# Kernel tuning notes

Hardware: AMD Instinct MI355X
Metric: run time of the kernel (lower is better)

The kernel has to match this reference:

```python
import jax, jax.numpy as jnp
import numpy as np

DIM = 1024
HEADS = 16
DIM_HEAD = 64
INNER = HEADS * DIM_HEAD  # 1024


def setup_inputs() -> dict:
    key = jax.random.key(0)
    k1, k2, k3, k4 = jax.random.split(key, 4)
    x = jax.random.normal(k1, (4, 2048, DIM), dtype=jnp.float32)
    # nn.Linear(dim, 3*inner, bias=False): weight (3*inner, dim); store transposed (dim, 3*inner)
    w_qkv = jax.random.normal(k2, (DIM, 3 * INNER), dtype=jnp.float32) * (DIM ** -0.5)
    # nn.Linear(inner, dim) with bias
    w_out = jax.random.normal(k3, (INNER, DIM), dtype=jnp.float32) * (INNER ** -0.5)
    b_out = jax.random.normal(k4, (DIM,), dtype=jnp.float32) * 0.01
    return {"x": x, "w_qkv": w_qkv, "w_out": w_out, "b_out": b_out}


def reference(x, w_qkv, w_out, b_out):
    b, n, _ = x.shape
    scale = DIM_HEAD ** -0.5
    qkv = x @ w_qkv  # [b, n, 3*inner]
    q, k, v = jnp.split(qkv, 3, axis=-1)
    # 'b n (h d) -> b h n d'
    def split_heads(t):
        return t.reshape(b, n, HEADS, DIM_HEAD).transpose(0, 2, 1, 3)
    q, k, v = split_heads(q), split_heads(k), split_heads(v)
    sim = jnp.einsum('bhid,bhjd->bhij', q, k) * scale  # [b, h, n, n]
    attn = jax.nn.softmax(sim, axis=-1)
    out = jnp.einsum('bhij,bhjd->bhid', attn, v)  # [b, h, n, d]
    out = out.transpose(0, 2, 1, 3).reshape(b, n, INNER)  # 'b h n d -> b n (h d)'
    return out @ w_out + b_out
```

## Files before the change

### kernel.cpp

```cpp
#include <hip/hip_runtime.h>
#include <hip/hip_bf16.h>

#define BATCH 4
#define SEQ   2048
#define DIM   1024
#define HEADS 16
#define DHEAD 64
#define INNER 1024
#define QKV_N 3072
#define MTOT  8192

typedef short bf16x8 __attribute__((ext_vector_type(8)));
typedef float f32x4  __attribute__((ext_vector_type(4)));
#define MFMA16(a,b,c) __builtin_amdgcn_mfma_f32_16x16x32_bf16((a),(b),(c),0,0,0)

#define QSCALE 0.1803368801111204f

static __device__ __forceinline__ unsigned fau(float f) { return __float_as_uint(f); }
static __device__ __forceinline__ float max3f(float a, float b, float c) {
    return fmaxf(fmaxf(a, b), c);
}

static __device__ __forceinline__ uint2 pack_hi4(float4 v) {
    return make_uint2((fau(v.x) >> 16) | (fau(v.y) & 0xffff0000u),
                      (fau(v.z) >> 16) | (fau(v.w) & 0xffff0000u));
}
static __device__ __forceinline__ float4 resid4(float4 v) {
    float4 r;
    r.x = v.x - __uint_as_float(fau(v.x) & 0xffff0000u);
    r.y = v.y - __uint_as_float(fau(v.y) & 0xffff0000u);
    r.z = v.z - __uint_as_float(fau(v.z) & 0xffff0000u);
    r.w = v.w - __uint_as_float(fau(v.w) & 0xffff0000u);
    return r;
}
static __device__ __forceinline__ uint2 pack_lo4(float4 v) { return pack_hi4(resid4(v)); }

static __device__ __forceinline__ unsigned cvt_pk_bf16(float a, float b) {
    unsigned r;
    asm("v_cvt_pk_bf16_f32 %0, %1, %2" : "=v"(r) : "v"(a), "v"(b));
    return r;
}

static __device__ __forceinline__ void barrier_lgkm() {
    asm volatile("s_waitcnt lgkmcnt(0)" ::: "memory");
    __builtin_amdgcn_s_barrier();
}

static __device__ __forceinline__ void stagger_block() {
    const unsigned flat = blockIdx.x + gridDim.x * (blockIdx.y + gridDim.y * blockIdx.z);
    const int slot = (int)(flat % 5u);
    #pragma unroll
    for (int i = 0; i < 4; ++i)
        if (i < slot) __builtin_amdgcn_s_sleep(6);
}

__global__ __launch_bounds__(256) void pack_rows_hl(const float* __restrict__ src,
                                                    unsigned short* __restrict__ dst,
                                                    int Mtot, int K)
{
    const int m = blockIdx.x * 256 + threadIdx.x;
    const int t = blockIdx.y;
    const float* sp = src + (size_t)m * K + t * 32;
    unsigned short buf[64];
    #pragma unroll
    for (int i = 0; i < 32; i += 4) {
        const float4 v = *(const float4*)&sp[i];
        *(uint2*)&buf[i]      = pack_hi4(v);
        *(uint2*)&buf[32 + i] = pack_lo4(v);
    }
    unsigned short* dp = dst + ((size_t)t * Mtot + m) * 64;
    const int s7 = m & 7;
    #pragma unroll
    for (int G = 0; G < 8; ++G)
        *(bf16x8*)&dp[(G ^ s7) * 8] = *(bf16x8*)&buf[G * 8];
}

__global__ __launch_bounds__(256) void pack_cols_hl(const float* __restrict__ src,
                                                    unsigned short* __restrict__ dst,
                                                    int Ntot)
{
    const int n = blockIdx.x * 256 + threadIdx.x;
    const int t = blockIdx.y;
    float vals[32];
    #pragma unroll
    for (int i = 0; i < 32; ++i) vals[i] = src[(size_t)(t * 32 + i) * Ntot + n];
    unsigned short buf[64];
    #pragma unroll
    for (int i = 0; i < 32; i += 4) {
        const float4 v = make_float4(vals[i], vals[i + 1], vals[i + 2], vals[i + 3]);
        *(uint2*)&buf[i]      = pack_hi4(v);
        *(uint2*)&buf[32 + i] = pack_lo4(v);
    }
    unsigned short* dp = dst + ((size_t)t * Ntot + n) * 64;
    const int s7 = n & 7;
    #pragma unroll
    for (int G = 0; G < 8; ++G)
        *(bf16x8*)&dp[(G ^ s7) * 8] = *(bf16x8*)&buf[G * 8];
}

static __device__ __forceinline__ void gemm_core_pk(const unsigned short* __restrict__ Ap,
                                                    const unsigned short* __restrict__ Bp,
                                                    unsigned short* As,
                                                    unsigned short* Bs,
                                                    f32x4 (&acc)[4][4],
                                                    int Mtot, int Ntot, int NT,
                                                    int row0, int col0)
{
    const int tid  = threadIdx.x;
    const int lane = tid & 63;
    const int w    = tid >> 6;
    const int l15  = lane & 15;
    const int g    = lane >> 4;
    const int wr   = w >> 1, wc = w & 1;

    const unsigned short* aSrc = Ap + (size_t)row0 * 64 + tid * 8;
    const unsigned short* bSrc = Bp + (size_t)col0 * 64 + tid * 8;
    const size_t aStep = (size_t)Mtot * 64;
    const size_t bStep = (size_t)Ntot * 64;

    int aoff[4][2], boff[4][2];
    #pragma unroll
    for (int mt = 0; mt < 4; ++mt) {
        const int m = wr * 64 + mt * 16 + l15;
        const int sw = (m & 7) << 3;
        aoff[mt][0] = m * 64 + ((g * 8) ^ sw);
        aoff[mt][1] = m * 64 + ((32 + g * 8) ^ sw);
    }
    #pragma unroll
    for (int nt = 0; nt < 4; ++nt) {
        const int n = wc * 64 + nt * 16 + l15;
        const int sw = (n & 7) << 3;
        boff[nt][0] = n * 64 + ((g * 8) ^ sw);
        boff[nt][1] = n * 64 + ((32 + g * 8) ^ sw);
    }

    bf16x8 ar[4], br[4];
    #pragma unroll
    for (int p = 0; p < 4; ++p) {
        ar[p] = *(const bf16x8*)(aSrc + p * 2048);
        br[p] = *(const bf16x8*)(bSrc + p * 2048);
    }
    #pragma unroll
    for (int p = 0; p < 4; ++p) {
        *(bf16x8*)&As[tid * 8 + p * 2048] = ar[p];
        *(bf16x8*)&Bs[tid * 8 + p * 2048] = br[p];
    }
    if (1 < NT) {
        #pragma unroll
        for (int p = 0; p < 4; ++p) {
            ar[p] = *(const bf16x8*)(aSrc + aStep + p * 2048);
            br[p] = *(const bf16x8*)(bSrc + bStep + p * 2048);
        }
    }
    __syncthreads();

    int cur = 0;
    for (int t = 0; t < NT; ++t) {
        const int cb = cur * 8192;
        bf16x8 ah[4], al[4], bh[4], bl[4];
        #pragma unroll
        for (int mt = 0; mt < 4; ++mt) {
            ah[mt] = *(const bf16x8*)&As[cb + aoff[mt][0]];
            al[mt] = *(const bf16x8*)&As[cb + aoff[mt][1]];
        }
        #pragma unroll
        for (int nt = 0; nt < 4; ++nt) {
            bh[nt] = *(const bf16x8*)&Bs[cb + boff[nt][0]];
            bl[nt] = *(const bf16x8*)&Bs[cb + boff[nt][1]];
        }
        if (t + 1 < NT) {
            const int nb = (cur ^ 1) * 8192;
            #pragma unroll
            for (int p = 0; p < 4; ++p) {
                *(bf16x8*)&As[nb + tid * 8 + p * 2048] = ar[p];
                *(bf16x8*)&Bs[nb + tid * 8 + p * 2048] = br[p];
            }
        }
        if (t + 2 < NT) {
            const unsigned short* a2 = aSrc + (size_t)(t + 2) * aStep;
            const unsigned short* b2 = bSrc + (size_t)(t + 2) * bStep;
            #pragma unroll
            for (int p = 0; p < 4; ++p) {
                ar[p] = *(const bf16x8*)(a2 + p * 2048);
                br[p] = *(const bf16x8*)(b2 + p * 2048);
            }
        }
        #pragma unroll
        for (int mt = 0; mt < 4; ++mt)
            #pragma unroll
            for (int nt = 0; nt < 4; ++nt) {
                acc[mt][nt] = MFMA16(ah[mt], bh[nt], acc[mt][nt]);
                acc[mt][nt] = MFMA16(ah[mt], bl[nt], acc[mt][nt]);
                acc[mt][nt] = MFMA16(al[mt], bh[nt], acc[mt][nt]);
            }
        barrier_lgkm();
        cur ^= 1;
    }
}

__global__ __launch_bounds__(256, 2) void gemm_out_pk(const unsigned short* __restrict__ Ap,
                                                      const unsigned short* __restrict__ Bp,
                                                      const float* __restrict__ bias,
                                                      float* __restrict__ C)
{
    __shared__ unsigned short As[2 * 128 * 64];
    __shared__ unsigned short Bs[2 * 128 * 64];

    stagger_block();

    const int tid  = threadIdx.x;
    const int lane = tid & 63;
    const int w    = tid >> 6;
    const int l15  = lane & 15;
    const int g    = lane >> 4;
    const int wr   = w >> 1, wc = w & 1;
    const int row0 = blockIdx.y * 128, col0 = blockIdx.x * 128;

    f32x4 acc[4][4] = {};
    gemm_core_pk(Ap, Bp, As, Bs, acc, MTOT, INNER, 32, row0, col0);

    #pragma unroll
    for (int nt = 0; nt < 4; ++nt) {
        const int c = col0 + wc * 64 + nt * 16 + l15;
        const float bv = bias[c];
        #pragma unroll
        for (int mt = 0; mt < 4; ++mt)
            #pragma unroll
            for (int r = 0; r < 4; ++r) {
                const int rr = row0 + wr * 64 + mt * 16 + g * 4 + r;
                C[(size_t)rr * INNER + c] = acc[mt][nt][r] + bv;
            }
    }
}

__global__ __launch_bounds__(256, 2) void gemm_qkv_pk(const unsigned short* __restrict__ Ap,
                                                      const unsigned short* __restrict__ Bp,
                                                      unsigned short* __restrict__ q_hl,
                                                      unsigned short* __restrict__ k_hl,
                                                      unsigned short* __restrict__ vt)
{
    __shared__ unsigned short As[2 * 128 * 64];
    __shared__ unsigned short Bs[2 * 128 * 64];

    stagger_block();

    const int tid  = threadIdx.x;
    const int lane = tid & 63;
    const int w    = tid >> 6;
    const int l15  = lane & 15;
    const int g    = lane >> 4;
    const int wr   = w >> 1, wc = w & 1;
    const int row0 = blockIdx.y * 128, col0 = blockIdx.x * 128;

    f32x4 acc[4][4] = {};
    gemm_core_pk(Ap, Bp, As, Bs, acc, MTOT, QKV_N, 32, row0, col0);

    if (col0 < 2 * INNER) {
        unsigned short* plane = (col0 < INNER) ? q_hl : k_hl;
        const float sc = (col0 < INNER) ? QSCALE : 1.0f;
        #pragma unroll
        for (int nt = 0; nt < 4; ++nt) {
            const int c  = col0 + wc * 64 + nt * 16 + l15;
            const int cc = c & (INNER - 1);
            const int hd = (cc >> 6) * 128 + (cc & 63);
            #pragma unroll
            for (int mt = 0; mt < 4; ++mt)
                #pragma unroll
                for (int r = 0; r < 4; ++r) {
                    const int rr = row0 + wr * 64 + mt * 16 + g * 4 + r;
                    const float v = acc[mt][nt][r] * sc;
                    const unsigned u = fau(v);
                    const float res = v - __uint_as_float(u & 0xffff0000u);
                    unsigned short* dp = plane + (size_t)rr * 2048 + hd;
                    dp[0]  = (unsigned short)(u >> 16);
                    dp[64] = (unsigned short)(fau(res) >> 16);
                }
        }
    } else {
        #pragma unroll
        for (int nt = 0; nt < 4; ++nt) {
            const int f = col0 + wc * 64 + nt * 16 + l15 - 2 * INNER;
            #pragma unroll
            for (int mt = 0; mt < 4; ++mt) {
                const int rr0 = row0 + wr * 64 + mt * 16 + g * 4;
                const int bb  = rr0 >> 11;
                const int n   = rr0 & (SEQ - 1);
                const int pn  = (n & ~31) | ((n & 12) << 1) | ((n & 16) >> 2);
                const uint2 pk = make_uint2(
                    cvt_pk_bf16(acc[mt][nt][0], acc[mt][nt][1]),
                    cvt_pk_bf16(acc[mt][nt][2], acc[mt][nt][3]));
                *(uint2*)&vt[((size_t)bb * INNER + f) * SEQ + pn] = pk;
            }
        }
    }
}

__global__ __launch_bounds__(256, 2) void attn_mfma(const unsigned short* __restrict__ q_hl,
                                                    const unsigned short* __restrict__ k_hl,
                                                    const unsigned short* __restrict__ vt,
                                                    unsigned short* __restrict__ ao_hl)
{
    __shared__ unsigned short Ks[2 * 64 * 128];
    __shared__ unsigned short Vs[2 * 64 * 64];

    stagger_block();

    const int tid  = threadIdx.x;
    const int lane = tid & 63;
    const int w    = tid >> 6;
    const int l15  = lane & 15;
    const int g    = lane >> 4;
    const int h  = blockIdx.x, qb = blockIdx.y, b = blockIdx.z;
    const int q0 = qb * 256 + w * 64;

    bf16x8 qh[4][2], ql[4][2];
    #pragma unroll
    for (int qs = 0; qs < 4; ++qs) {
        const unsigned short* qp =
            q_hl + (size_t)(b * SEQ + q0 + qs * 16 + l15) * 2048 + h * 128;
        #pragma unroll
        for (int kk = 0; kk < 2; ++kk) {
            qh[qs][kk] = *(const bf16x8*)&qp[kk * 32 + g * 8];
            ql[qs][kk] = *(const bf16x8*)&qp[64 + kk * 32 + g * 8];
        }
    }

    f32x4 o[4][4] = {};
    float m_run[4] = {-1e30f, -1e30f, -1e30f, -1e30f};
    float l_run[4] = {0.f, 0.f, 0.f, 0.f};

    const int kj   = tid >> 4;
    const int ko8  = (tid & 15) * 8;
    const int kdst = kj * 128 + (ko8 ^ (kj << 3));
    const unsigned short* ksrc =
        k_hl + ((size_t)(b * SEQ + kj)) * 2048 + h * 128 + ko8;

    const int vd   = tid >> 3;
    const int vu8  = (tid & 7) * 8;
    const int vdst = vd * 64 + (vu8 ^ ((vd & 7) << 3));
    const unsigned short* vsrc =
        vt + ((size_t)(b * HEADS + h) * 64 + vd) * SEQ + vu8;

    const int krow = l15 * 128;
    int koff[2][2];
    #pragma unroll
    for (int kk = 0; kk < 2; ++kk) {
        koff[kk][0] = (kk * 32 + g * 8) ^ (l15 * 8);
        koff[kk][1] = (64 + kk * 32 + g * 8) ^ (l15 * 8);
    }
    const int vrow = l15 * 64;
    const int voff[2] = { (g * 8) ^ ((l15 & 7) * 8), (32 + g * 8) ^ ((l15 & 7) * 8) };

    bf16x8 kr[4], vr[2];
    #pragma unroll
    for (int p = 0; p < 4; ++p)
        kr[p] = *(const bf16x8*)&ksrc[(size_t)(p * 16) * 2048];
    #pragma unroll
    for (int p = 0; p < 2; ++p)
        vr[p] = *(const bf16x8*)&vsrc[(size_t)p * 32 * SEQ];

    int cur = 0;
    for (int kv = 0; kv < SEQ / 64; ++kv) {
        const int kb = cur * 8192, vb = cur * 4096;
        #pragma unroll
        for (int p = 0; p < 4; ++p)
            *(bf16x8*)&Ks[kb + p * 2048 + kdst] = kr[p];
        #pragma unroll
        for (int p = 0; p < 2; ++p)
            *(bf16x8*)&Vs[vb + p * 2048 + vdst] = vr[p];
        barrier_lgkm();
        if (kv + 1 < SEQ / 64) {
            const int j0n = (kv + 1) * 64;
            #pragma unroll
            for (int p = 0; p < 4; ++p)
                kr[p] = *(const bf16x8*)&ksrc[(size_t)(j0n + p * 16) * 2048];
            #pragma unroll
            for (int p = 0; p < 2; ++p)
                vr[p] = *(const bf16x8*)&vsrc[(size_t)p * 32 * SEQ + j0n];
        }

        f32x4 s[4][4] = {};
        __builtin_amdgcn_s_setprio(1);
        #pragma unroll
        for (int jt = 0; jt < 4; ++jt) {
            #pragma unroll
            for (int kk = 0; kk < 2; ++kk) {
                const bf16x8 khf = *(const bf16x8*)&Ks[kb + jt * 2048 + krow + koff[kk][0]];
                const bf16x8 klf = *(const bf16x8*)&Ks[kb + jt * 2048 + krow + koff[kk][1]];
                #pragma unroll
                for (int qs = 0; qs < 4; ++qs) {
                    s[qs][jt] = MFMA16(khf, qh[qs][kk], s[qs][jt]);
                    s[qs][jt] = MFMA16(khf, ql[qs][kk], s[qs][jt]);
                    s[qs][jt] = MFMA16(klf, qh[qs][kk], s[qs][jt]);
                }
            }
        }
        __builtin_amdgcn_s_setprio(0);

        bf16x8 pav[4][2];
        #pragma unroll
        for (int qs = 0; qs < 4; ++qs) {
            const f32x4* sq = s[qs];
            float mx = max3f(sq[0][0], sq[0][1], sq[0][2]);
            mx = max3f(mx, sq[0][3], sq[1][0]);
            mx = max3f(mx, sq[1][1], sq[1][2]);
            mx = max3f(mx, sq[1][3], sq[2][0]);
            mx = max3f(mx, sq[2][1], sq[2][2]);
            mx = max3f(mx, sq[2][3], sq[3][0]);
            mx = max3f(mx, sq[3][1], sq[3][2]);
            mx = fmaxf(mx, sq[3][3]);
            mx = fmaxf(mx, __shfl_xor(mx, 16));
            mx = fmaxf(mx, __shfl_xor(mx, 32));
            if (!__all(mx - m_run[qs] <= 8.f)) {
                const float mnew = fmaxf(m_run[qs], mx);
                const float corr = __builtin_amdgcn_exp2f(m_run[qs] - mnew);
                m_run[qs] = mnew;
                l_run[qs] *= corr;
                const float cr0 = __shfl(corr, g * 4 + 0);
                const float cr1 = __shfl(corr, g * 4 + 1);
                const float cr2 = __shfl(corr, g * 4 + 2);
                const float cr3 = __shfl(corr, g * 4 + 3);
                #pragma unroll
                for (int nt = 0; nt < 4; ++nt) {
                    o[qs][nt][0] *= cr0; o[qs][nt][1] *= cr1;
                    o[qs][nt][2] *= cr2; o[qs][nt][3] *= cr3;
                }
            }
            float sm = 0.f;
            #pragma unroll
            for (int jt = 0; jt < 4; ++jt)
                #pragma unroll
                for (int r = 0; r < 4; ++r) {
                    const float e = __builtin_amdgcn_exp2f(s[qs][jt][r] - m_run[qs]);
                    s[qs][jt][r] = e; sm += e;
                }
            sm += __shfl_xor(sm, 16);
            sm += __shfl_xor(sm, 32);
            l_run[qs] += sm;

            #pragma unroll
            for (int t = 0; t < 2; ++t) {
                union { uint2 u[2]; bf16x8 v; } P;
                P.u[0] = make_uint2(cvt_pk_bf16(s[qs][2 * t][0],     s[qs][2 * t][1]),
                                    cvt_pk_bf16(s[qs][2 * t][2],     s[qs][2 * t][3]));
                P.u[1] = make_uint2(cvt_pk_bf16(s[qs][2 * t + 1][0], s[qs][2 * t + 1][1]),
                                    cvt_pk_bf16(s[qs][2 * t + 1][2], s[qs][2 * t + 1][3]));
                pav[qs][t] = P.v;
            }
        }

        __builtin_amdgcn_s_setprio(1);
        #pragma unroll
        for (int t = 0; t < 2; ++t)
            #pragma unroll
            for (int nt = 0; nt < 4; ++nt) {
                const bf16x8 vbv = *(const bf16x8*)&Vs[vb + nt * 1024 + vrow + voff[t]];
                #pragma unroll
                for (int qs = 0; qs < 4; ++qs)
                    o[qs][nt] = MFMA16(pav[qs][t], vbv, o[qs][nt]);
            }
        __builtin_amdgcn_s_setprio(0);
        cur ^= 1;
    }

    #pragma unroll
    for (int qs = 0; qs < 4; ++qs) {
        const float il = 1.f / l_run[qs];
        const float nr0 = __shfl(il, g * 4 + 0);
        const float nr1 = __shfl(il, g * 4 + 1);
        const float nr2 = __shfl(il, g * 4 + 2);
        const float nr3 = __shfl(il, g * 4 + 3);
        const float nr[4] = {nr0, nr1, nr2, nr3};
        #pragma unroll
        for (int nt = 0; nt < 4; ++nt) {
            const int k  = h * DHEAD + nt * 16 + l15;
            const int t  = k >> 5;
            const int kk = k & 31;
            const int G  = kk >> 3;
            const int e  = kk & 7;
            #pragma unroll
            for (int r = 0; r < 4; ++r) {
                const int M  = b * SEQ + q0 + qs * 16 + g * 4 + r;
                const int s7 = M & 7;
                unsigned short* dp = ao_hl + ((size_t)t * MTOT + M) * 64;
                const float v = o[qs][nt][r] * nr[r];
                const unsigned u = fau(v);
                const float res = v - __uint_as_float(u & 0xffff0000u);
                dp[((G ^ s7) << 3) + e]       = (unsigned short)(u >> 16);
                dp[(((G + 4) ^ s7) << 3) + e] = (unsigned short)(fau(res) >> 16);
            }
        }
    }
}

extern "C" void kernel_launch(void* const* d_in, const int* in_sizes, int n_in,
                              void* d_out, int out_size, void* d_ws, size_t ws_size,
                              hipStream_t stream)
{
    const float* x     = (const float*)d_in[0];
    const float* w_qkv = (const float*)d_in[1];
    const float* w_out = (const float*)d_in[2];
    const float* b_out = (const float*)d_in[3];
    float* out = (float*)d_out;

    unsigned short* q_hl  = (unsigned short*)d_ws;
    unsigned short* k_hl  = q_hl  + (size_t)MTOT * 2048;
    unsigned short* vt    = k_hl  + (size_t)MTOT * 2048;
    unsigned short* xa_hl = vt    + (size_t)BATCH * INNER * SEQ;
    unsigned short* wq_hl = xa_hl + (size_t)32 * MTOT * 64;
    unsigned short* wo_hl = wq_hl + (size_t)32 * QKV_N * 64;

    pack_rows_hl<<<dim3(MTOT / 256, 32), 256, 0, stream>>>(x, xa_hl, MTOT, DIM);
    pack_cols_hl<<<dim3(QKV_N / 256, 32), 256, 0, stream>>>(w_qkv, wq_hl, QKV_N);
    pack_cols_hl<<<dim3(INNER / 256, 32), 256, 0, stream>>>(w_out, wo_hl, INNER);

    gemm_qkv_pk<<<dim3(QKV_N / 128, MTOT / 128), 256, 0, stream>>>(
        xa_hl, wq_hl, q_hl, k_hl, vt);

    attn_mfma<<<dim3(HEADS, SEQ / 256, BATCH), 256, 0, stream>>>(
        q_hl, k_hl, vt, xa_hl);

    gemm_out_pk<<<dim3(INNER / 128, MTOT / 128), 256, 0, stream>>>(
        xa_hl, wo_hl, b_out, out);
}
```

Measured before the change: 350.5 us.

## Use 256x128 tiles with 8 waves in QKV and output GEMMs

```diff
diff --git a/kernel.cpp b/kernel.cpp
--- a/kernel.cpp
+++ b/kernel.cpp
@@ -98,115 +98,145 @@
         *(bf16x8*)&dp[(G ^ s7) * 8] = *(bf16x8*)&buf[G * 8];
 }
 
-static __device__ __forceinline__ void gemm_core_pk(const unsigned short* __restrict__ Ap,
-                                                    const unsigned short* __restrict__ Bp,
-                                                    unsigned short* As,
-                                                    unsigned short* Bs,
-                                                    f32x4 (&acc)[4][4],
-                                                    int Mtot, int Ntot, int NT,
-                                                    int row0, int col0)
-{
+static __device__ __forceinline__ void gemm_core_pk8(const unsigned short* __restrict__ Ap,
+                                                     const unsigned short* __restrict__ Bp,
+                                                     unsigned short* As,
+                                                     unsigned short* Bs,
+                                                     f32x4 (&acc)[4][4],
+                                                     int Mtot, int Ntot, int NT,
+                                                     int row0, int col0)
+{
+    const int tid  = threadIdx.x;
+    const int lane = tid & 63;
+    const int w    = tid >> 6;
+    const int l15  = lane & 15;
+    const int g    = lane >> 4;
+    const int wr   = w >> 1;
+    const int wc   = w & 1;
+
+    const unsigned short* aSrc = Ap + (size_t)row0 * 64 + tid * 8;
+    const unsigned short* bSrc = Bp + (size_t)col0 * 64 + tid * 8;
+    const size_t aStep = (size_t)Mtot * 64;
+    const size_t bStep = (size_t)Ntot * 64;
+
+    int aoff[4][2], boff[4][2];
+    #pragma unroll
+    for (int mt = 0; mt < 4; ++mt) {
+        const int m = wr * 64 + mt * 16 + l15;
+        const int sw = (m & 7) << 3;
+        aoff[mt][0] = m * 64 + ((g * 8) ^ sw);
+        aoff[mt][1] = m * 64 + ((32 + g * 8) ^ sw);
+    }
+    #pragma unroll
+    for (int nt = 0; nt < 4; ++nt) {
+        const int n = wc * 64 + nt * 16 + l15;
+        const int sw = (n & 7) << 3;
+        boff[nt][0] = n * 64 + ((g * 8) ^ sw);
+        boff[nt][1] = n * 64 + ((32 + g * 8) ^ sw);
+    }
+
+    bf16x8 ar[4], br[2];
+    #pragma unroll
+    for (int p = 0; p < 4; ++p) ar[p] = *(const bf16x8*)(aSrc + p * 4096);
+    #pragma unroll
+    for (int p = 0; p < 2; ++p) br[p] = *(const bf16x8*)(bSrc + p * 4096);
+    #pragma unroll
+    for (int p = 0; p < 4; ++p) *(bf16x8*)&As[tid * 8 + p * 4096] = ar[p];
+    #pragma unroll
+    for (int p = 0; p < 2; ++p) *(bf16x8*)&Bs[tid * 8 + p * 4096] = br[p];
+    if (1 < NT) {
+        #pragma unroll
+        for (int p = 0; p < 4; ++p) ar[p] = *(const bf16x8*)(aSrc + aStep + p * 4096);
+        #pragma unroll
+        for (int p = 0; p < 2; ++p) br[p] = *(const bf16x8*)(bSrc + bStep + p * 4096);
+    }
+    __syncthreads();
+
+    int cur = 0;
+    for (int t = 0; t < NT; ++t) {
+        const int ca = cur * 16384, cb = cur * 8192;
+        bf16x8 ah[4], al[4], bh[4], bl[4];
+        #pragma unroll
+        for (int mt = 0; mt < 4; ++mt) {
+            ah[mt] = *(const bf16x8*)&As[ca + aoff[mt][0]];
+            al[mt] = *(const bf16x8*)&As[ca + aoff[mt][1]];
+        }
+        #pragma unroll
+        for (int nt = 0; nt < 4; ++nt) {
+            bh[nt] = *(const bf16x8*)&Bs[cb + boff[nt][0]];
+            bl[nt] = *(const bf16x8*)&Bs[cb + boff[nt][1]];
+        }
+        if (t + 1 < NT) {
+            const int na = (cur ^ 1) * 16384, nb = (cur ^ 1) * 8192;
+            #pragma unroll
+            for (int p = 0; p < 4; ++p)
+                *(bf16x8*)&As[na + tid * 8 + p * 4096] = ar[p];
+            #pragma unroll
+            for (int p = 0; p < 2; ++p)
+                *(bf16x8*)&Bs[nb + tid * 8 + p * 4096] = br[p];
+        }
+        if (t + 2 < NT) {
+            const unsigned short* a2 = aSrc + (size_t)(t + 2) * aStep;
+            const unsigned short* b2 = bSrc + (size_t)(t + 2) * bStep;
+            #pragma unroll
+            for (int p = 0; p < 4; ++p) ar[p] = *(const bf16x8*)(a2 + p * 4096);
+            #pragma unroll
+            for (int p = 0; p < 2; ++p) br[p] = *(const bf16x8*)(b2 + p * 4096);
+        }
+        #pragma unroll
+        for (int mt = 0; mt < 4; ++mt)
+            #pragma unroll
+            for (int nt = 0; nt < 4; ++nt) {
+                acc[mt][nt] = MFMA16(ah[mt], bh[nt], acc[mt][nt]);
+                acc[mt][nt] = MFMA16(ah[mt], bl[nt], acc[mt][nt]);
+                acc[mt][nt] = MFMA16(al[mt], bh[nt], acc[mt][nt]);
+            }
+        barrier_lgkm();
+        cur ^= 1;
+    }
+}
+
+__global__ __launch_bounds__(512, 2) void gemm_out_pk(const unsigned short* __restrict__ Ap,
+                                                      const unsigned short* __restrict__ Bp,
+                                                      const float* __restrict__ bias,
+                                                      float* __restrict__ C)
+{
+    __shared__ unsigned short As[2 * 256 * 64];
+    __shared__ unsigned short Bs[2 * 128 * 64];
+
     const int tid  = threadIdx.x;
     const int lane = tid & 63;
     const int w    = tid >> 6;
     const int l15  = lane & 15;
     const int g    = lane >> 4;
     const int wr   = w >> 1, wc = w & 1;
-
-    const unsigned short* aSrc = Ap + (size_t)row0 * 64 + tid * 8;
-    const unsigned short* bSrc = Bp + (size_t)col0 * 64 + tid * 8;
-    const size_t aStep = (size_t)Mtot * 64;
-    const size_t bStep = (size_t)Ntot * 64;
-
-    int aoff[4][2], boff[4][2];
-    #pragma unroll
-    for (int mt = 0; mt < 4; ++mt) {
-        const int m = wr * 64 + mt * 16 + l15;
-        const int sw = (m & 7) << 3;
-        aoff[mt][0] = m * 64 + ((g * 8) ^ sw);
-        aoff[mt][1] = m * 64 + ((32 + g * 8) ^ sw);
-    }
+    const int row0 = blockIdx.y * 256, col0 = blockIdx.x * 128;
+
+    f32x4 acc[4][4] = {};
+    gemm_core_pk8(Ap, Bp, As, Bs, acc, MTOT, INNER, 32, row0, col0);
+
     #pragma unroll
     for (int nt = 0; nt < 4; ++nt) {
-        const int n = wc * 64 + nt * 16 + l15;
-        const int sw = (n & 7) << 3;
-        boff[nt][0] = n * 64 + ((g * 8) ^ sw);
-        boff[nt][1] = n * 64 + ((32 + g * 8) ^ sw);
-    }
-
-    bf16x8 ar[4], br[4];
-    #pragma unroll
-    for (int p = 0; p < 4; ++p) {
-        ar[p] = *(const bf16x8*)(aSrc + p * 2048);
-        br[p] = *(const bf16x8*)(bSrc + p * 2048);
-    }
-    #pragma unroll
-    for (int p = 0; p < 4; ++p) {
-        *(bf16x8*)&As[tid * 8 + p * 2048] = ar[p];
-        *(bf16x8*)&Bs[tid * 8 + p * 2048] = br[p];
-    }
-    if (1 < NT) {
-        #pragma unroll
-        for (int p = 0; p < 4; ++p) {
-            ar[p] = *(const bf16x8*)(aSrc + aStep + p * 2048);
-            br[p] = *(const bf16x8*)(bSrc + bStep + p * 2048);
-        }
-    }
-    __syncthreads();
-
-    int cur = 0;
-    for (int t = 0; t < NT; ++t) {
-        const int cb = cur * 8192;
-        bf16x8 ah[4], al[4], bh[4], bl[4];
-        #pragma unroll
-        for (int mt = 0; mt < 4; ++mt) {
-            ah[mt] = *(const bf16x8*)&As[cb + aoff[mt][0]];
-            al[mt] = *(const bf16x8*)&As[cb + aoff[mt][1]];
-        }
-        #pragma unroll
-        for (int nt = 0; nt < 4; ++nt) {
-            bh[nt] = *(const bf16x8*)&Bs[cb + boff[nt][0]];
-            bl[nt] = *(const bf16x8*)&Bs[cb + boff[nt][1]];
-        }
-        if (t + 1 < NT) {
-            const int nb = (cur ^ 1) * 8192;
-            #pragma unroll
-            for (int p = 0; p < 4; ++p) {
-                *(bf16x8*)&As[nb + tid * 8 + p * 2048] = ar[p];
-                *(bf16x8*)&Bs[nb + tid * 8 + p * 2048] = br[p];
-            }
-        }
-        if (t + 2 < NT) {
-            const unsigned short* a2 = aSrc + (size_t)(t + 2) * aStep;
-            const unsigned short* b2 = bSrc + (size_t)(t + 2) * bStep;
-            #pragma unroll
-            for (int p = 0; p < 4; ++p) {
-                ar[p] = *(const bf16x8*)(a2 + p * 2048);
-                br[p] = *(const bf16x8*)(b2 + p * 2048);
-            }
-        }
+        const int c = col0 + wc * 64 + nt * 16 + l15;
+        const float bv = bias[c];
         #pragma unroll
         for (int mt = 0; mt < 4; ++mt)
             #pragma unroll
-            for (int nt = 0; nt < 4; ++nt) {
-                acc[mt][nt] = MFMA16(ah[mt], bh[nt], acc[mt][nt]);
-                acc[mt][nt] = MFMA16(ah[mt], bl[nt], acc[mt][nt]);
-                acc[mt][nt] = MFMA16(al[mt], bh[nt], acc[mt][nt]);
-            }
-        barrier_lgkm();
-        cur ^= 1;
-    }
-}
-
-__global__ __launch_bounds__(256, 2) void gemm_out_pk(const unsigned short* __restrict__ Ap,
+            for (int r = 0; r < 4; ++r) {
+                const int rr = row0 + wr * 64 + mt * 16 + g * 4 + r;
+                C[(size_t)rr * INNER + c] = acc[mt][nt][r] + bv;
+            }
+    }
+}
+
+__global__ __launch_bounds__(512, 2) void gemm_qkv_pk(const unsigned short* __restrict__ Ap,
                                                       const unsigned short* __restrict__ Bp,
-                                                      const float* __restrict__ bias,
-                                                      float* __restrict__ C)
-{
-    __shared__ unsigned short As[2 * 128 * 64];
+                                                      unsigned short* __restrict__ q_hl,
+                                                      unsigned short* __restrict__ k_hl,
+                                                      unsigned short* __restrict__ vt)
+{
+    __shared__ unsigned short As[2 * 256 * 64];
     __shared__ unsigned short Bs[2 * 128 * 64];
-
-    stagger_block();
 
     const int tid  = threadIdx.x;
     const int lane = tid & 63;
@@ -214,46 +244,10 @@
     const int l15  = lane & 15;
     const int g    = lane >> 4;
     const int wr   = w >> 1, wc = w & 1;
-    const int row0 = blockIdx.y * 128, col0 = blockIdx.x * 128;
+    const int row0 = blockIdx.y * 256, col0 = blockIdx.x * 128;
 
     f32x4 acc[4][4] = {};
-    gemm_core_pk(Ap, Bp, As, Bs, acc, MTOT, INNER, 32, row0, col0);
-
-    #pragma unroll
-    for (int nt = 0; nt < 4; ++nt) {
-        const int c = col0 + wc * 64 + nt * 16 + l15;
-        const float bv = bias[c];
-        #pragma unroll
-        for (int mt = 0; mt < 4; ++mt)
-            #pragma unroll
-            for (int r = 0; r < 4; ++r) {
-                const int rr = row0 + wr * 64 + mt * 16 + g * 4 + r;
-                C[(size_t)rr * INNER + c] = acc[mt][nt][r] + bv;
-            }
-    }
-}
-
-__global__ __launch_bounds__(256, 2) void gemm_qkv_pk(const unsigned short* __restrict__ Ap,
-                                                      const unsigned short* __restrict__ Bp,
-                                                      unsigned short* __restrict__ q_hl,
-                                                      unsigned short* __restrict__ k_hl,
-                                                      unsigned short* __restrict__ vt)
-{
-    __shared__ unsigned short As[2 * 128 * 64];
-    __shared__ unsigned short Bs[2 * 128 * 64];
-
-    stagger_block();
-
-    const int tid  = threadIdx.x;
-    const int lane = tid & 63;
-    const int w    = tid >> 6;
-    const int l15  = lane & 15;
-    const int g    = lane >> 4;
-    const int wr   = w >> 1, wc = w & 1;
-    const int row0 = blockIdx.y * 128, col0 = blockIdx.x * 128;
-
-    f32x4 acc[4][4] = {};
-    gemm_core_pk(Ap, Bp, As, Bs, acc, MTOT, QKV_N, 32, row0, col0);
+    gemm_core_pk8(Ap, Bp, As, Bs, acc, MTOT, QKV_N, 32, row0, col0);
 
     if (col0 < 2 * INNER) {
         unsigned short* plane = (col0 < INNER) ? q_hl : k_hl;
@@ -514,12 +508,12 @@
     pack_cols_hl<<<dim3(QKV_N / 256, 32), 256, 0, stream>>>(w_qkv, wq_hl, QKV_N);
     pack_cols_hl<<<dim3(INNER / 256, 32), 256, 0, stream>>>(w_out, wo_hl, INNER);
 
-    gemm_qkv_pk<<<dim3(QKV_N / 128, MTOT / 128), 256, 0, stream>>>(
+    gemm_qkv_pk<<<dim3(QKV_N / 128, MTOT / 256), 512, 0, stream>>>(
         xa_hl, wq_hl, q_hl, k_hl, vt);
 
     attn_mfma<<<dim3(HEADS, SEQ / 256, BATCH), 256, 0, stream>>>(
         q_hl, k_hl, vt, xa_hl);
 
-    gemm_out_pk<<<dim3(INNER / 128, MTOT / 128), 256, 0, stream>>>(
+    gemm_out_pk<<<dim3(INNER / 128, MTOT / 256), 512, 0, stream>>>(
         xa_hl, wo_hl, b_out, out);
 }
```

Result: faster. 341.9 us, median of 2 (-2.4%).
